# Kernel optimization log

Measured on AMD Instinct MI355X. Metric: run time of the kernel, lower is better.

## Reference

```python
import jax, jax.numpy as jnp
import numpy as np

N_NODES = 100000


def gcn_conv(x, edge_src, edge_dst, W, b):
    # PyG GCNConv: h = x @ W; add self-loops; symmetric normalization; scatter-add; + bias
    n = x.shape[0]
    h = x @ W  # [N, out]
    loop = jnp.arange(n, dtype=edge_src.dtype)
    src = jnp.concatenate([edge_src, loop])
    dst = jnp.concatenate([edge_dst, loop])
    deg = jax.ops.segment_sum(jnp.ones_like(dst, dtype=h.dtype), dst, num_segments=n)
    dinv = jnp.where(deg > 0, jax.lax.rsqrt(deg), 0.0)
    norm = dinv[src] * dinv[dst]  # [E+N]
    msg = h[src] * norm[:, None]  # gather + scale
    out = jax.ops.segment_sum(msg, dst, num_segments=n)  # scatter-add
    return out + b


def setup_inputs() -> dict:
    key = jax.random.key(0)
    ks = jax.random.split(key, 12)
    F_in, H, H2, C = 128, 64, 32, 2
    x = jax.random.normal(ks[0], (N_NODES, F_in), dtype=jnp.float32)
    edge_index = jax.random.randint(ks[1], (2, 3200000), 0, N_NODES, dtype=jnp.int64)
    def glorot(k, shape):
        lim = float(np.sqrt(6.0 / (shape[0] + shape[1])))
        return jax.random.uniform(k, shape, jnp.float32, -lim, lim)
    return {
        "x": x,
        "edge_index": edge_index,
        "W1": glorot(ks[2], (F_in, H)), "b1": jnp.zeros((H,), jnp.float32),
        "W2": glorot(ks[3], (H, H)), "b2": jnp.zeros((H,), jnp.float32),
        "Wl1": glorot(ks[4], (H, H2)), "bl1": jnp.zeros((H2,), jnp.float32),
        "Wl2": glorot(ks[5], (H2, C)), "bl2": jnp.zeros((C,), jnp.float32),
    }


def reference(x, edge_index, W1, b1, W2, b2, Wl1, bl1, Wl2, bl2):
    src, dst = edge_index[0], edge_index[1]
    h = gcn_conv(x, src, dst, W1, b1)
    h = jax.nn.relu(h)
    # dropout is identity in eval mode (training=self.training)
    h = gcn_conv(h, src, dst, W2, b2)
    h = h @ Wl1 + bl1
    h = h @ Wl2 + bl2
    return jax.nn.softmax(h, axis=0)
```

## Files before the change

### kernel.cpp

```cpp
#include <hip/hip_runtime.h>

#define F_IN 128
#define NBMAX 512
#define TILE1 8192
#define CAP   9472
#define CAP2  10240

typedef __attribute__((ext_vector_type(8))) short short8;
typedef __attribute__((ext_vector_type(4))) float f32x4;
typedef __attribute__((ext_vector_type(2))) float f32x2;

__device__ __forceinline__ unsigned short f2bf(float f) {
    unsigned u = __float_as_uint(f);
    u += 0x7fffu + ((u >> 16) & 1u);
    return (unsigned short)(u >> 16);
}

__device__ __forceinline__ unsigned char f2fp8(float f) {
    return (unsigned char)(__builtin_amdgcn_cvt_pk_fp8_f32(f, f, 0, false) & 0xff);
}

__device__ __forceinline__ unsigned ldG(const unsigned* __restrict__ G,
                                        unsigned c, unsigned sl) {
    return *(const unsigned*)((const char*)G + ((c << 6) + (sl << 2)));
}

__global__ __launch_bounds__(1024) void k_part1(const int* __restrict__ src,
                                                const int* __restrict__ dst,
                                                int* __restrict__ cursor,
                                                unsigned* __restrict__ ebuf,
                                                int E, int nb) {
    __shared__ unsigned staged[TILE1];
    __shared__ unsigned short sbuck[TILE1];
    __shared__ int hist[NBMAX], lbase[NBMAX], lcur[NBMAX], gbase[NBMAX];
    int t = threadIdx.x;
    for (int i = t; i < nb; i += 1024) hist[i] = 0;
    __syncthreads();
    int base = blockIdx.x * TILE1;
    int end = min(base + TILE1, E);
    for (int i = base + t; i < end; i += 1024)
        atomicAdd(&hist[dst[i] >> 8], 1);
    __syncthreads();
    if (t < 64) {
        int carry = 0;
        for (int c = 0; c < (nb + 63) / 64; ++c) {
            int idx = c * 64 + t;
            int v = (idx < nb) ? hist[idx] : 0;
            int inc = v;
            for (int d = 1; d < 64; d <<= 1) {
                int u = __shfl_up(inc, d, 64);
                if (t >= d) inc += u;
            }
            if (idx < nb) { int ex = carry + inc - v; lbase[idx] = ex; lcur[idx] = ex; }
            carry += __shfl(inc, 63, 64);
        }
    }
    __syncthreads();
    for (int i = t; i < nb; i += 1024)
        gbase[i] = i * CAP + (hist[i] ? atomicAdd(&cursor[i], hist[i]) : 0);
    for (int i = base + t; i < end; i += 1024) {
        int d = dst[i];
        int b = d >> 8;
        int r = atomicAdd(&lcur[b], 1);
        staged[r] = ((unsigned)src[i] << 8) | (unsigned)(d & 255);
        sbuck[r] = (unsigned short)b;
    }
    __syncthreads();
    int cnt = end - base;
    for (int i = t; i < cnt; i += 1024) {
        int b = sbuck[i];
        __builtin_nontemporal_store(staged[i], &ebuf[gbase[b] + (i - lbase[b])]);
    }
}

__global__ __launch_bounds__(1024) void k_part2(const unsigned* __restrict__ ebuf,
                                                const int* __restrict__ cursor,
                                                int* __restrict__ csr,
                                                uint2* __restrict__ offs2,
                                                float* __restrict__ dinv, int n) {
    __shared__ unsigned staged[CAP2];
    __shared__ int hist[256], lcur[256];
    int t = threadIdx.x;
    int b = blockIdx.x;
    int beg = b * CAP;
    int cnt = cursor[b];
    int end = beg + cnt;
    if (t < 256) hist[t] = 0;
    __syncthreads();
    for (int i = beg + t; i < end; i += 1024)
        atomicAdd(&hist[ebuf[i] & 255u], 1);
    __syncthreads();
    if (t < 64) {
        int carry = 0;
        for (int c = 0; c < 4; ++c) {
            int idx = c * 64 + t;
            int v = hist[idx];
            int inc = v;
            for (int d = 1; d < 64; d <<= 1) {
                int u = __shfl_up(inc, d, 64);
                if (t >= d) inc += u;
            }
            int ex = carry + inc - v;
            lcur[idx] = ex;
            int node = b * 256 + idx;
            if (node < n) {
                offs2[node] = make_uint2((unsigned)(beg + ex), (unsigned)(beg + ex + v));
                dinv[node] = rsqrtf((float)(v + 1));
            }
            carry += __shfl(inc, 63, 64);
        }
    }
    __syncthreads();
    for (int i = beg + t; i < end; i += 1024) {
        unsigned e = __builtin_nontemporal_load(ebuf + i);
        int r = atomicAdd(&lcur[(int)(e & 255u)], 1);
        staged[r] = e >> 8;
    }
    __syncthreads();
    for (int i = t; i < cnt; i += 1024)
        csr[beg + i] = (int)staged[i];
    if (t < 64) csr[end + t] = n;
}

template<int K, bool INBF16>
__global__ __launch_bounds__(256) void k_gemm_mfma(const void* __restrict__ Xv,
                                                   const float* __restrict__ W,
                                                   const float* __restrict__ dinv,
                                                   unsigned* __restrict__ G, int n,
                                                   const float* __restrict__ W2,
                                                   const float* __restrict__ b2,
                                                   const float* __restrict__ Wl1,
                                                   const float* __restrict__ bl1,
                                                   const float* __restrict__ Wl2,
                                                   const float* __restrict__ bl2,
                                                   float* __restrict__ Wfold,
                                                   float* __restrict__ bconst) {
    constexpr int AST = K + 8;
    __shared__ unsigned short A_lds[64 * AST];
    __shared__ unsigned short Wt_lds[64 * AST];
    __shared__ unsigned char C8[64 * 68];
    __shared__ float Wc[64][2];
    __shared__ float bc0[2];
    int t = threadIdx.x;
    int base = blockIdx.x * 64;

    if (blockIdx.x == 0) {
        if (t < 128) {
            int k = t >> 1, c = t & 1;
            float s = 0.f;
            for (int m = 0; m < 32; ++m) s += Wl1[k * 32 + m] * Wl2[m * 2 + c];
            Wc[k][c] = s;
        } else if (t < 130) {
            int c = t - 128;
            float s = bl2[c];
            for (int m = 0; m < 32; ++m) s += bl1[m] * Wl2[m * 2 + c];
            bc0[c] = s;
        } else if (t >= 240 && t < 256) {
            G[(size_t)n * 16 + (t - 240)] = 0u;
        }
        __syncthreads();
        if (t < 128) {
            int k = t >> 1, c = t & 1;
            float s = 0.f;
            for (int j = 0; j < 64; ++j) s += W2[k * 64 + j] * Wc[j][c];
            Wfold[k * 2 + c] = s;
        } else if (t < 130) {
            int c = t - 128;
            float s = bc0[c];
            for (int j = 0; j < 64; ++j) s += b2[j] * Wc[j][c];
            bconst[c] = s;
        }
    }

    for (int idx = t; idx < K * 64; idx += 256) {
        int k = idx >> 6, nn = idx & 63;
        Wt_lds[nn * AST + k] = f2bf(W[idx]);
    }
    if (!INBF16) {
        const f32x4* X4 = (const f32x4*)Xv;
        constexpr int F4 = K / 4;
        for (int idx = t; idx < 64 * F4; idx += 256) {
            int row = idx / F4, c4 = idx % F4;
            f32x4 f = {0.f, 0.f, 0.f, 0.f};
            if (base + row < n) f = X4[(size_t)base * F4 + idx];
            unsigned p0 = (unsigned)f2bf(f.x) | ((unsigned)f2bf(f.y) << 16);
            unsigned p1 = (unsigned)f2bf(f.z) | ((unsigned)f2bf(f.w) << 16);
            *(uint2*)&A_lds[row * AST + c4 * 4] = make_uint2(p0, p1);
        }
    } else {
        const unsigned* H32 = (const unsigned*)Xv;
        constexpr int U2 = K / 2;
        for (int idx = t; idx < 64 * U2; idx += 256) {
            int row = idx / U2, c2 = idx % U2;
            unsigned u = 0;
            if (base + row < n) u = H32[(size_t)base * U2 + idx];
            *(unsigned*)&A_lds[row * AST + c2 * 2] = u;
        }
    }
    __syncthreads();

    int lane = t & 63, w = t >> 6;
    int q = lane >> 4, m = lane & 15;
    f32x4 acc0 = {0,0,0,0}, acc1 = {0,0,0,0}, acc2 = {0,0,0,0}, acc3 = {0,0,0,0};
    const unsigned short* arow = &A_lds[(16 * w + m) * AST + q * 8];
#pragma unroll
    for (int s = 0; s < K / 32; ++s) {
        short8 a  = *(const short8*)(arow + s * 32);
        short8 w0 = *(const short8*)&Wt_lds[ m       * AST + s * 32 + q * 8];
        short8 w1 = *(const short8*)&Wt_lds[(16 + m) * AST + s * 32 + q * 8];
        short8 w2 = *(const short8*)&Wt_lds[(32 + m) * AST + s * 32 + q * 8];
        short8 w3 = *(const short8*)&Wt_lds[(48 + m) * AST + s * 32 + q * 8];
        acc0 = __builtin_amdgcn_mfma_f32_16x16x32_bf16(a, w0, acc0, 0, 0, 0);
        acc1 = __builtin_amdgcn_mfma_f32_16x16x32_bf16(a, w1, acc1, 0, 0, 0);
        acc2 = __builtin_amdgcn_mfma_f32_16x16x32_bf16(a, w2, acc2, 0, 0, 0);
        acc3 = __builtin_amdgcn_mfma_f32_16x16x32_bf16(a, w3, acc3, 0, 0, 0);
    }
    float dv[4];
#pragma unroll
    for (int r = 0; r < 4; ++r) {
        int node = base + 16 * w + q * 4 + r;
        dv[r] = (node < n) ? dinv[node] : 0.f;
    }
#pragma unroll
    for (int r = 0; r < 4; ++r) {
        int row = 16 * w + q * 4 + r;
        C8[row * 68 + m]      = f2fp8(acc0[r] * dv[r]);
        C8[row * 68 + 16 + m] = f2fp8(acc1[r] * dv[r]);
        C8[row * 68 + 32 + m] = f2fp8(acc2[r] * dv[r]);
        C8[row * 68 + 48 + m] = f2fp8(acc3[r] * dv[r]);
    }
    __syncthreads();
    for (int idx = t; idx < 1024; idx += 256) {
        int row = idx >> 4, c4 = idx & 15;
        int node = base + row;
        if (node < n) G[(size_t)node * 16 + c4] = *(const unsigned*)&C8[row * 68 + c4 * 4];
    }
}

__global__ __launch_bounds__(256) void k_gfold(const int* __restrict__ csr,
                                               const uint2* __restrict__ offs2,
                                               const unsigned* __restrict__ G,
                                               const float* __restrict__ dinv,
                                               const float* __restrict__ bias,
                                               const float* __restrict__ Wfold,
                                               float2* __restrict__ P, int n) {
    int w = (blockIdx.x * 256 + threadIdx.x) >> 6;
    if (w >= n) return;
    int lane = threadIdx.x & 63;
    unsigned g = (unsigned)lane >> 4, sl = (unsigned)lane & 15u;
    uint2 o = offs2[w];
    int beg = (int)o.x, end = (int)o.y;
    f32x2 A01 = {0.f, 0.f}, A23 = {0.f, 0.f};

    unsigned selfU = ldG(G, (unsigned)w, sl);
    for (int e = beg; e < end; e += 64) {
        int i0 = e + (int)g;
        int vv[16];
#pragma unroll
        for (int k = 0; k < 16; ++k)
            vv[k] = csr[i0 + 4 * k];
        unsigned uu[16];
#pragma unroll
        for (int k = 0; k < 16; ++k) {
            unsigned c = (i0 + 4 * k < end) ? (unsigned)vv[k] : (unsigned)n;
            uu[k] = ldG(G, c, sl);
        }
#pragma unroll
        for (int k = 0; k < 16; ++k) {
            A01 += __builtin_amdgcn_cvt_pk_f32_fp8((int)uu[k], false);
            A23 += __builtin_amdgcn_cvt_pk_f32_fp8((int)uu[k], true);
        }
    }
    float a0 = A01.x, a1 = A01.y, a2 = A23.x, a3 = A23.y;
    a0 += __shfl_xor(a0, 16, 64); a1 += __shfl_xor(a1, 16, 64);
    a2 += __shfl_xor(a2, 16, 64); a3 += __shfl_xor(a3, 16, 64);
    a0 += __shfl_xor(a0, 32, 64); a1 += __shfl_xor(a1, 32, 64);
    a2 += __shfl_xor(a2, 32, 64); a3 += __shfl_xor(a3, 32, 64);
    A01 = __builtin_amdgcn_cvt_pk_f32_fp8((int)selfU, false);
    A23 = __builtin_amdgcn_cvt_pk_f32_fp8((int)selfU, true);
    a0 += A01.x; a1 += A01.y; a2 += A23.x; a3 += A23.y;
    float d = dinv[w];
    float4 bb = ((const float4*)bias)[sl];
    float v0 = fmaxf(fmaf(a0, d, bb.x), 0.f);
    float v1 = fmaxf(fmaf(a1, d, bb.y), 0.f);
    float v2 = fmaxf(fmaf(a2, d, bb.z), 0.f);
    float v3 = fmaxf(fmaf(a3, d, bb.w), 0.f);
    float4 wa = ((const float4*)Wfold)[2 * sl];
    float4 wb = ((const float4*)Wfold)[2 * sl + 1];
    float px = v0 * wa.x + v1 * wa.z + v2 * wb.x + v3 * wb.z;
    float py = v0 * wa.y + v1 * wa.w + v2 * wb.y + v3 * wb.w;
    px += __shfl_xor(px, 1, 64); py += __shfl_xor(py, 1, 64);
    px += __shfl_xor(px, 2, 64); py += __shfl_xor(py, 2, 64);
    px += __shfl_xor(px, 4, 64); py += __shfl_xor(py, 4, 64);
    px += __shfl_xor(px, 8, 64); py += __shfl_xor(py, 8, 64);
    if (lane == 0) P[w] = make_float2(px * d, py * d);
}

__global__ __launch_bounds__(256) void k_gather2(const int* __restrict__ csr,
                                                 const uint2* __restrict__ offs2,
                                                 const float2* __restrict__ P,
                                                 const float* __restrict__ dinv,
                                                 const float* __restrict__ bconst,
                                                 float* __restrict__ logits, int n) {
    int w = (blockIdx.x * 256 + threadIdx.x) >> 4;
    if (w >= n) return;
    int sl = threadIdx.x & 15;
    uint2 o = offs2[w];
    int beg = (int)o.x, end = (int)o.y;
    float ax = 0.f, ay = 0.f;
    for (int e = beg; e < end; e += 64) {
        int i0 = e + sl;
        int vv[4];
#pragma unroll
        for (int k = 0; k < 4; ++k)
            vv[k] = csr[i0 + 16 * k];
#pragma unroll
        for (int k = 0; k < 4; ++k) {
            unsigned j = (i0 + 16 * k < end) ? (unsigned)vv[k] : (unsigned)n;
            float2 p = *(const float2*)((const char*)P + (j << 3));
            ax += p.x; ay += p.y;
        }
    }
    ax += __shfl_xor(ax, 1, 64); ay += __shfl_xor(ay, 1, 64);
    ax += __shfl_xor(ax, 2, 64); ay += __shfl_xor(ay, 2, 64);
    ax += __shfl_xor(ax, 4, 64); ay += __shfl_xor(ay, 4, 64);
    ax += __shfl_xor(ax, 8, 64); ay += __shfl_xor(ay, 8, 64);
    if (sl == 0) {
        float2 self = P[w];
        float d = dinv[w];
        logits[w * 2]     = d * (self.x + ax) + bconst[0];
        logits[w * 2 + 1] = d * (self.y + ay) + bconst[1];
    }
}

__global__ __launch_bounds__(256) void k_sm_part(const float* __restrict__ logits,
                                                 float4* __restrict__ partials, int n) {
    __shared__ float r0[256], r1[256];
    int t = threadIdx.x;
    int i = blockIdx.x * 256 + t;
    float l0 = -3.4e38f, l1 = -3.4e38f;
    if (i < n) { l0 = logits[i * 2]; l1 = logits[i * 2 + 1]; }
    r0[t] = l0; r1[t] = l1;
    __syncthreads();
    for (int s = 128; s > 0; s >>= 1) {
        if (t < s) { r0[t] = fmaxf(r0[t], r0[t + s]); r1[t] = fmaxf(r1[t], r1[t + s]); }
        __syncthreads();
    }
    float m0 = r0[0], m1 = r1[0];
    __syncthreads();
    r0[t] = (i < n) ? __expf(l0 - m0) : 0.f;
    r1[t] = (i < n) ? __expf(l1 - m1) : 0.f;
    __syncthreads();
    for (int s = 128; s > 0; s >>= 1) {
        if (t < s) { r0[t] += r0[t + s]; r1[t] += r1[t + s]; }
        __syncthreads();
    }
    if (t == 0) partials[blockIdx.x] = make_float4(m0, r0[0], m1, r1[0]);
}

__global__ __launch_bounds__(256) void k_sm_final(const float* __restrict__ logits,
                                                  const float4* __restrict__ partials,
                                                  float* __restrict__ out, int n, int nbp) {
    __shared__ float m0s[256], s0s[256], m1s[256], s1s[256];
    int t = threadIdx.x;
    float m0 = -3.4e38f, s0 = 0.f, m1 = -3.4e38f, s1 = 0.f;
    for (int i = t; i < nbp; i += 256) {
        float4 p = partials[i];
        float M = fmaxf(m0, p.x);
        s0 = s0 * __expf(m0 - M) + p.y * __expf(p.x - M); m0 = M;
        M = fmaxf(m1, p.z);
        s1 = s1 * __expf(m1 - M) + p.w * __expf(p.z - M); m1 = M;
    }
    m0s[t] = m0; s0s[t] = s0; m1s[t] = m1; s1s[t] = s1;
    __syncthreads();
    for (int s = 128; s > 0; s >>= 1) {
        if (t < s) {
            float Ma = m0s[t], Mb = m0s[t + s];
            float M = fmaxf(Ma, Mb);
            s0s[t] = s0s[t] * __expf(Ma - M) + s0s[t + s] * __expf(Mb - M);
            m0s[t] = M;
            Ma = m1s[t]; Mb = m1s[t + s];
            M = fmaxf(Ma, Mb);
            s1s[t] = s1s[t] * __expf(Ma - M) + s1s[t + s] * __expf(Mb - M);
            m1s[t] = M;
        }
        __syncthreads();
    }
    float M0 = m0s[0], inv0 = 1.f / s0s[0];
    float M1 = m1s[0], inv1 = 1.f / s1s[0];
    int i = blockIdx.x * 256 + t;
    if (i < n) {
        out[i * 2]     = __expf(logits[i * 2]     - M0) * inv0;
        out[i * 2 + 1] = __expf(logits[i * 2 + 1] - M1) * inv1;
    }
}

extern "C" void kernel_launch(void* const* d_in, const int* in_sizes, int n_in,
                              void* d_out, int out_size, void* d_ws, size_t ws_size,
                              hipStream_t stream) {
    const float* x   = (const float*)d_in[0];
    const int*   ei  = (const int*)d_in[1];
    const float* W1  = (const float*)d_in[2];
    const float* b1  = (const float*)d_in[3];
    const float* W2  = (const float*)d_in[4];
    const float* b2  = (const float*)d_in[5];
    const float* Wl1 = (const float*)d_in[6];
    const float* bl1 = (const float*)d_in[7];
    const float* Wl2 = (const float*)d_in[8];
    const float* bl2 = (const float*)d_in[9];
    float* out = (float*)d_out;

    int N = in_sizes[0] / F_IN;
    int E = in_sizes[1] / 2;
    const int* esrc = ei;
    const int* edst = ei + E;

    int nbuck = (N + 255) / 256;

    char* ws = (char*)d_ws;
    size_t off = 0;
    auto alloc = [&](size_t bytes) { void* p = ws + off; off += (bytes + 255) & ~(size_t)255; return p; };
    int*            cursor = (int*)alloc((size_t)NBMAX * 4);
    float*          dinv   = (float*)alloc((size_t)N * 4);
    uint2*          offs2  = (uint2*)alloc((size_t)N * 8);
    int*            csr    = (int*)alloc((size_t)nbuck * CAP * 4);
    unsigned*       ebuf   = (unsigned*)alloc((size_t)nbuck * CAP * 4);
    unsigned*       gbuf   = (unsigned*)alloc((size_t)(N + 1) * 64);
    float*          Wfold  = (float*)alloc(64 * 2 * 4);
    float*          bconst = (float*)alloc(2 * 4);
    float2*         P      = (float2*)alloc((size_t)(N + 1) * 8);
    float*          logits = (float*)alloc((size_t)N * 2 * 4);
    float4*         smpart = (float4*)alloc((size_t)NBMAX * 16);

    hipMemsetAsync(cursor, 0, NBMAX * sizeof(int), stream);
    hipMemsetAsync(P + N, 0, sizeof(float2), stream);

    int tiles = (E + TILE1 - 1) / TILE1;
    int mb = (N + 63) / 64;
    int wb = (N * 64 + 255) / 256;
    int qb = (N * 16 + 255) / 256;
    int nb = (N + 255) / 256;

    k_part1<<<tiles, 1024, 0, stream>>>(esrc, edst, cursor, ebuf, E, nbuck);
    k_part2<<<nbuck, 1024, 0, stream>>>(ebuf, cursor, csr, offs2, dinv, N);

    k_gemm_mfma<128, false><<<mb, 256, 0, stream>>>(x, W1, dinv, gbuf, N,
                                                    W2, b2, Wl1, bl1, Wl2, bl2,
                                                    Wfold, bconst);

    k_gfold<<<wb, 256, 0, stream>>>(csr, offs2, gbuf, dinv, b1, Wfold, P, N);

    k_gather2<<<qb, 256, 0, stream>>>(csr, offs2, P, dinv, bconst, logits, N);

    k_sm_part<<<nb, 256, 0, stream>>>(logits, smpart, N);
    k_sm_final<<<nb, 256, 0, stream>>>(logits, smpart, out, N, nb);
}
```

Baseline: 223.9 us.

## Pad CSR rows to multiples of 64 with sentinel indices to drop bounds checks

Result: slower. 232.0 us (+3.6%).

```diff
diff --git a/kernel.cpp b/kernel.cpp
--- a/kernel.cpp
+++ b/kernel.cpp
@@ -4,7 +4,7 @@
 #define NBMAX 512
 #define TILE1 8192
 #define CAP   9472
-#define CAP2  10240
+#define CAPC  16896
 
 typedef __attribute__((ext_vector_type(8))) short short8;
 typedef __attribute__((ext_vector_type(4))) float f32x4;
@@ -78,11 +78,13 @@
                                                 int* __restrict__ csr,
                                                 uint2* __restrict__ offs2,
                                                 float* __restrict__ dinv, int n) {
-    __shared__ unsigned staged[CAP2];
+    __shared__ int staged[CAPC];
     __shared__ int hist[256], lcur[256];
+    __shared__ int sh_ptot;
     int t = threadIdx.x;
     int b = blockIdx.x;
     int beg = b * CAP;
+    int cbase = b * CAPC;
     int cnt = cursor[b];
     int end = beg + cnt;
     if (t < 256) hist[t] = 0;
@@ -95,31 +97,37 @@
         for (int c = 0; c < 4; ++c) {
             int idx = c * 64 + t;
             int v = hist[idx];
-            int inc = v;
+            int pd = (v + 63) & ~63;
+            int inc = pd;
             for (int d = 1; d < 64; d <<= 1) {
                 int u = __shfl_up(inc, d, 64);
                 if (t >= d) inc += u;
             }
-            int ex = carry + inc - v;
+            int ex = carry + inc - pd;
             lcur[idx] = ex;
             int node = b * 256 + idx;
             if (node < n) {
-                offs2[node] = make_uint2((unsigned)(beg + ex), (unsigned)(beg + ex + v));
+                offs2[node] = make_uint2((unsigned)(cbase + ex),
+                                         (unsigned)(cbase + ex + pd));
                 dinv[node] = rsqrtf((float)(v + 1));
             }
             carry += __shfl(inc, 63, 64);
         }
-    }
-    __syncthreads();
+        if (t == 0) sh_ptot = carry;
+    } else {
+        for (int i = t - 64; i < CAPC; i += 960) staged[i] = n;
+    }
+    __syncthreads();
+    if (t < 64) {  }
     for (int i = beg + t; i < end; i += 1024) {
         unsigned e = __builtin_nontemporal_load(ebuf + i);
         int r = atomicAdd(&lcur[(int)(e & 255u)], 1);
-        staged[r] = e >> 8;
-    }
-    __syncthreads();
-    for (int i = t; i < cnt; i += 1024)
-        csr[beg + i] = (int)staged[i];
-    if (t < 64) csr[end + t] = n;
+        staged[r] = (int)(e >> 8);
+    }
+    __syncthreads();
+    int ptot = sh_ptot;
+    for (int i = t; i < ptot; i += 1024)
+        csr[cbase + i] = staged[i];
 }
 
 template<int K, bool INBF16>
@@ -249,22 +257,16 @@
     int lane = threadIdx.x & 63;
     unsigned g = (unsigned)lane >> 4, sl = (unsigned)lane & 15u;
     uint2 o = offs2[w];
-    int beg = (int)o.x, end = (int)o.y;
+    int beg = (int)o.x, pend = (int)o.y;
     f32x2 A01 = {0.f, 0.f}, A23 = {0.f, 0.f};
 
     unsigned selfU = ldG(G, (unsigned)w, sl);
-    for (int e = beg; e < end; e += 64) {
+    for (int e = beg; e < pend; e += 64) {
         int i0 = e + (int)g;
-        int vv[16];
+        unsigned uu[16];
 #pragma unroll
         for (int k = 0; k < 16; ++k)
-            vv[k] = csr[i0 + 4 * k];
-        unsigned uu[16];
-#pragma unroll
-        for (int k = 0; k < 16; ++k) {
-            unsigned c = (i0 + 4 * k < end) ? (unsigned)vv[k] : (unsigned)n;
-            uu[k] = ldG(G, c, sl);
-        }
+            uu[k] = ldG(G, (unsigned)csr[i0 + 4 * k], sl);
 #pragma unroll
         for (int k = 0; k < 16; ++k) {
             A01 += __builtin_amdgcn_cvt_pk_f32_fp8((int)uu[k], false);
@@ -306,17 +308,13 @@
     if (w >= n) return;
     int sl = threadIdx.x & 15;
     uint2 o = offs2[w];
-    int beg = (int)o.x, end = (int)o.y;
+    int beg = (int)o.x, pend = (int)o.y;
     float ax = 0.f, ay = 0.f;
-    for (int e = beg; e < end; e += 64) {
+    for (int e = beg; e < pend; e += 64) {
         int i0 = e + sl;
-        int vv[4];
-#pragma unroll
-        for (int k = 0; k < 4; ++k)
-            vv[k] = csr[i0 + 16 * k];
 #pragma unroll
         for (int k = 0; k < 4; ++k) {
-            unsigned j = (i0 + 16 * k < end) ? (unsigned)vv[k] : (unsigned)n;
+            unsigned j = (unsigned)csr[i0 + 16 * k];
             float2 p = *(const float2*)((const char*)P + (j << 3));
             ax += p.x; ay += p.y;
         }
@@ -423,7 +421,7 @@
     int*            cursor = (int*)alloc((size_t)NBMAX * 4);
     float*          dinv   = (float*)alloc((size_t)N * 4);
     uint2*          offs2  = (uint2*)alloc((size_t)N * 8);
-    int*            csr    = (int*)alloc((size_t)nbuck * CAP * 4);
+    int*            csr    = (int*)alloc((size_t)nbuck * CAPC * 4);
     unsigned*       ebuf   = (unsigned*)alloc((size_t)nbuck * CAP * 4);
     unsigned*       gbuf   = (unsigned*)alloc((size_t)(N + 1) * 64);
     float*          Wfold  = (float*)alloc(64 * 2 * 4);
```

## Shrink partition buckets and fuse softmax partial reduction into gather kernel

Applied to the files above, without the earlier changes.

New measurement: 241.5 us. +7.9%, slower.

```diff
diff --git a/kernel.cpp b/kernel.cpp
--- a/kernel.cpp
+++ b/kernel.cpp
@@ -1,10 +1,9 @@
 #include <hip/hip_runtime.h>
 
 #define F_IN 128
-#define NBMAX 512
-#define TILE1 8192
-#define CAP   9472
-#define CAP2  10240
+#define NBMAX 1024
+#define TILE1 4096
+#define CAPB  4800
 
 typedef __attribute__((ext_vector_type(8))) short short8;
 typedef __attribute__((ext_vector_type(4))) float f32x4;
@@ -25,21 +24,28 @@
     return *(const unsigned*)((const char*)G + ((c << 6) + (sl << 2)));
 }
 
-__global__ __launch_bounds__(1024) void k_part1(const int* __restrict__ src,
-                                                const int* __restrict__ dst,
-                                                int* __restrict__ cursor,
-                                                unsigned* __restrict__ ebuf,
-                                                int E, int nb) {
+__global__ __launch_bounds__(512) void k_part1(const int* __restrict__ src,
+                                               const int* __restrict__ dst,
+                                               int* __restrict__ cursor,
+                                               unsigned* __restrict__ ebuf,
+                                               int E, int nb) {
     __shared__ unsigned staged[TILE1];
     __shared__ unsigned short sbuck[TILE1];
     __shared__ int hist[NBMAX], lbase[NBMAX], lcur[NBMAX], gbase[NBMAX];
     int t = threadIdx.x;
-    for (int i = t; i < nb; i += 1024) hist[i] = 0;
+    for (int i = t; i < nb; i += 512) hist[i] = 0;
     __syncthreads();
     int base = blockIdx.x * TILE1;
     int end = min(base + TILE1, E);
-    for (int i = base + t; i < end; i += 1024)
-        atomicAdd(&hist[dst[i] >> 8], 1);
+    int dreg[8];
+#pragma unroll
+    for (int k = 0; k < 8; ++k) {
+        int i = base + t + 512 * k;
+        dreg[k] = (i < end) ? dst[i] : -1;
+    }
+#pragma unroll
+    for (int k = 0; k < 8; ++k)
+        if (dreg[k] >= 0) atomicAdd(&hist[dreg[k] >> 7], 1);
     __syncthreads();
     if (t < 64) {
         int carry = 0;
@@ -56,43 +62,46 @@
         }
     }
     __syncthreads();
-    for (int i = t; i < nb; i += 1024)
-        gbase[i] = i * CAP + (hist[i] ? atomicAdd(&cursor[i], hist[i]) : 0);
-    for (int i = base + t; i < end; i += 1024) {
-        int d = dst[i];
-        int b = d >> 8;
-        int r = atomicAdd(&lcur[b], 1);
-        staged[r] = ((unsigned)src[i] << 8) | (unsigned)(d & 255);
-        sbuck[r] = (unsigned short)b;
+    for (int i = t; i < nb; i += 512)
+        gbase[i] = i * CAPB + (hist[i] ? atomicAdd(&cursor[i], hist[i]) : 0);
+#pragma unroll
+    for (int k = 0; k < 8; ++k) {
+        if (dreg[k] < 0) continue;
+        int i = base + t + 512 * k;
+        int d = dreg[k];
+        int bb = d >> 7;
+        int r = atomicAdd(&lcur[bb], 1);
+        staged[r] = ((unsigned)src[i] << 8) | (unsigned)(d & 127);
+        sbuck[r] = (unsigned short)bb;
     }
     __syncthreads();
     int cnt = end - base;
-    for (int i = t; i < cnt; i += 1024) {
-        int b = sbuck[i];
-        __builtin_nontemporal_store(staged[i], &ebuf[gbase[b] + (i - lbase[b])]);
-    }
-}
-
-__global__ __launch_bounds__(1024) void k_part2(const unsigned* __restrict__ ebuf,
-                                                const int* __restrict__ cursor,
-                                                int* __restrict__ csr,
-                                                uint2* __restrict__ offs2,
-                                                float* __restrict__ dinv, int n) {
-    __shared__ unsigned staged[CAP2];
-    __shared__ int hist[256], lcur[256];
+    for (int i = t; i < cnt; i += 512) {
+        int bb = sbuck[i];
+        ebuf[gbase[bb] + (i - lbase[bb])] = staged[i];
+    }
+}
+
+__global__ __launch_bounds__(512) void k_part2(const unsigned* __restrict__ ebuf,
+                                               const int* __restrict__ cursor,
+                                               int* __restrict__ csr,
+                                               uint2* __restrict__ offs2,
+                                               float* __restrict__ dinv, int n) {
+    __shared__ int staged[CAPB];
+    __shared__ int hist[128], lcur[128];
     int t = threadIdx.x;
     int b = blockIdx.x;
-    int beg = b * CAP;
+    int beg = b * CAPB;
     int cnt = cursor[b];
     int end = beg + cnt;
-    if (t < 256) hist[t] = 0;
-    __syncthreads();
-    for (int i = beg + t; i < end; i += 1024)
-        atomicAdd(&hist[ebuf[i] & 255u], 1);
+    if (t < 128) hist[t] = 0;
+    __syncthreads();
+    for (int i = beg + t; i < end; i += 512)
+        atomicAdd(&hist[ebuf[i] & 127u], 1);
     __syncthreads();
     if (t < 64) {
         int carry = 0;
-        for (int c = 0; c < 4; ++c) {
+        for (int c = 0; c < 2; ++c) {
             int idx = c * 64 + t;
             int v = hist[idx];
             int inc = v;
@@ -102,7 +111,7 @@
             }
             int ex = carry + inc - v;
             lcur[idx] = ex;
-            int node = b * 256 + idx;
+            int node = b * 128 + idx;
             if (node < n) {
                 offs2[node] = make_uint2((unsigned)(beg + ex), (unsigned)(beg + ex + v));
                 dinv[node] = rsqrtf((float)(v + 1));
@@ -111,14 +120,14 @@
         }
     }
     __syncthreads();
-    for (int i = beg + t; i < end; i += 1024) {
-        unsigned e = __builtin_nontemporal_load(ebuf + i);
-        int r = atomicAdd(&lcur[(int)(e & 255u)], 1);
-        staged[r] = e >> 8;
-    }
-    __syncthreads();
-    for (int i = t; i < cnt; i += 1024)
-        csr[beg + i] = (int)staged[i];
+    for (int i = beg + t; i < end; i += 512) {
+        unsigned e = ebuf[i];
+        int r = atomicAdd(&lcur[(int)(e & 127u)], 1);
+        staged[r] = (int)(e >> 8);
+    }
+    __syncthreads();
+    for (int i = t; i < cnt; i += 512)
+        csr[beg + i] = staged[i];
     if (t < 64) csr[end + t] = n;
 }
 
@@ -301,11 +310,15 @@
                                                  const float2* __restrict__ P,
                                                  const float* __restrict__ dinv,
                                                  const float* __restrict__ bconst,
-                                                 float* __restrict__ logits, int n) {
-    int w = (blockIdx.x * 256 + threadIdx.x) >> 4;
-    if (w >= n) return;
-    int sl = threadIdx.x & 15;
-    uint2 o = offs2[w];
+                                                 float* __restrict__ logits,
+                                                 float4* __restrict__ partials, int n) {
+    __shared__ float sml[16][2];
+    int t = threadIdx.x;
+    int w = (blockIdx.x * 256 + t) >> 4;
+    int sl = t & 15;
+    int grp = t >> 4;
+    bool valid = (w < n);
+    uint2 o = valid ? offs2[w] : make_uint2(0u, 0u);
     int beg = (int)o.x, end = (int)o.y;
     float ax = 0.f, ay = 0.f;
     for (int e = beg; e < end; e += 64) {
@@ -325,37 +338,34 @@
     ax += __shfl_xor(ax, 2, 64); ay += __shfl_xor(ay, 2, 64);
     ax += __shfl_xor(ax, 4, 64); ay += __shfl_xor(ay, 4, 64);
     ax += __shfl_xor(ax, 8, 64); ay += __shfl_xor(ay, 8, 64);
-    if (sl == 0) {
+    float l0 = -3.4e38f, l1 = -3.4e38f;
+    if (valid && sl == 0) {
         float2 self = P[w];
         float d = dinv[w];
-        logits[w * 2]     = d * (self.x + ax) + bconst[0];
-        logits[w * 2 + 1] = d * (self.y + ay) + bconst[1];
-    }
-}
-
-__global__ __launch_bounds__(256) void k_sm_part(const float* __restrict__ logits,
-                                                 float4* __restrict__ partials, int n) {
-    __shared__ float r0[256], r1[256];
-    int t = threadIdx.x;
-    int i = blockIdx.x * 256 + t;
-    float l0 = -3.4e38f, l1 = -3.4e38f;
-    if (i < n) { l0 = logits[i * 2]; l1 = logits[i * 2 + 1]; }
-    r0[t] = l0; r1[t] = l1;
-    __syncthreads();
-    for (int s = 128; s > 0; s >>= 1) {
-        if (t < s) { r0[t] = fmaxf(r0[t], r0[t + s]); r1[t] = fmaxf(r1[t], r1[t + s]); }
-        __syncthreads();
-    }
-    float m0 = r0[0], m1 = r1[0];
-    __syncthreads();
-    r0[t] = (i < n) ? __expf(l0 - m0) : 0.f;
-    r1[t] = (i < n) ? __expf(l1 - m1) : 0.f;
-    __syncthreads();
-    for (int s = 128; s > 0; s >>= 1) {
-        if (t < s) { r0[t] += r0[t + s]; r1[t] += r1[t + s]; }
-        __syncthreads();
-    }
-    if (t == 0) partials[blockIdx.x] = make_float4(m0, r0[0], m1, r1[0]);
+        l0 = d * (self.x + ax) + bconst[0];
+        l1 = d * (self.y + ay) + bconst[1];
+        logits[w * 2]     = l0;
+        logits[w * 2 + 1] = l1;
+    }
+    if (sl == 0) { sml[grp][0] = l0; sml[grp][1] = l1; }
+    __syncthreads();
+    if (t < 16) {
+        float a = sml[t][0], bv = sml[t][1];
+        float m0 = a, m1 = bv;
+#pragma unroll
+        for (int d = 1; d < 16; d <<= 1) {
+            m0 = fmaxf(m0, __shfl_xor(m0, d, 64));
+            m1 = fmaxf(m1, __shfl_xor(m1, d, 64));
+        }
+        float e0 = (a > -1e38f) ? __expf(a - m0) : 0.f;
+        float e1 = (bv > -1e38f) ? __expf(bv - m1) : 0.f;
+#pragma unroll
+        for (int d = 1; d < 16; d <<= 1) {
+            e0 += __shfl_xor(e0, d, 64);
+            e1 += __shfl_xor(e1, d, 64);
+        }
+        if (t == 0) partials[blockIdx.x] = make_float4(m0, e0, m1, e1);
+    }
 }
 
 __global__ __launch_bounds__(256) void k_sm_final(const float* __restrict__ logits,
@@ -415,7 +425,7 @@
     const int* esrc = ei;
     const int* edst = ei + E;
 
-    int nbuck = (N + 255) / 256;
+    int nbuck = (N + 127) / 128;
 
     char* ws = (char*)d_ws;
     size_t off = 0;
@@ -423,14 +433,15 @@
     int*            cursor = (int*)alloc((size_t)NBMAX * 4);
     float*          dinv   = (float*)alloc((size_t)N * 4);
     uint2*          offs2  = (uint2*)alloc((size_t)N * 8);
-    int*            csr    = (int*)alloc((size_t)nbuck * CAP * 4);
-    unsigned*       ebuf   = (unsigned*)alloc((size_t)nbuck * CAP * 4);
+    int*            csr    = (int*)alloc((size_t)nbuck * CAPB * 4);
+    unsigned*       ebuf   = (unsigned*)alloc((size_t)nbuck * CAPB * 4);
     unsigned*       gbuf   = (unsigned*)alloc((size_t)(N + 1) * 64);
     float*          Wfold  = (float*)alloc(64 * 2 * 4);
     float*          bconst = (float*)alloc(2 * 4);
     float2*         P      = (float2*)alloc((size_t)(N + 1) * 8);
     float*          logits = (float*)alloc((size_t)N * 2 * 4);
-    float4*         smpart = (float4*)alloc((size_t)NBMAX * 16);
+    int qb = (N * 16 + 255) / 256;
+    float4*         partials = (float4*)alloc((size_t)qb * 16);
 
     hipMemsetAsync(cursor, 0, NBMAX * sizeof(int), stream);
     hipMemsetAsync(P + N, 0, sizeof(float2), stream);
@@ -438,11 +449,10 @@
     int tiles = (E + TILE1 - 1) / TILE1;
     int mb = (N + 63) / 64;
     int wb = (N * 64 + 255) / 256;
-    int qb = (N * 16 + 255) / 256;
     int nb = (N + 255) / 256;
 
-    k_part1<<<tiles, 1024, 0, stream>>>(esrc, edst, cursor, ebuf, E, nbuck);
-    k_part2<<<nbuck, 1024, 0, stream>>>(ebuf, cursor, csr, offs2, dinv, N);
+    k_part1<<<tiles, 512, 0, stream>>>(esrc, edst, cursor, ebuf, E, nbuck);
+    k_part2<<<nbuck, 512, 0, stream>>>(ebuf, cursor, csr, offs2, dinv, N);
 
     k_gemm_mfma<128, false><<<mb, 256, 0, stream>>>(x, W1, dinv, gbuf, N,
                                                     W2, b2, Wl1, bl1, Wl2, bl2,
@@ -450,8 +460,7 @@
 
     k_gfold<<<wb, 256, 0, stream>>>(csr, offs2, gbuf, dinv, b1, Wfold, P, N);
 
-    k_gather2<<<qb, 256, 0, stream>>>(csr, offs2, P, dinv, bconst, logits, N);
-
-    k_sm_part<<<nb, 256, 0, stream>>>(logits, smpart, N);
-    k_sm_final<<<nb, 256, 0, stream>>>(logits, smpart, out, N, nb);
-}
+    k_gather2<<<qb, 256, 0, stream>>>(csr, offs2, P, dinv, bconst, logits, partials, N);
+
+    k_sm_final<<<nb, 256, 0, stream>>>(logits, partials, out, N, qb);
+}
```

## Split layer-1 gather into two feature halves and fuse softmax partials into gather2

Applied to the files above, without the earlier changes.

Result: slower. 257.4 us (+15.0%).

```diff
diff --git a/kernel.cpp b/kernel.cpp
--- a/kernel.cpp
+++ b/kernel.cpp
@@ -15,14 +15,16 @@
     u += 0x7fffu + ((u >> 16) & 1u);
     return (unsigned short)(u >> 16);
 }
+__device__ __forceinline__ float bflo(unsigned u) { return __uint_as_float(u << 16); }
+__device__ __forceinline__ float bfhi(unsigned u) { return __uint_as_float(u & 0xffff0000u); }
 
 __device__ __forceinline__ unsigned char f2fp8(float f) {
     return (unsigned char)(__builtin_amdgcn_cvt_pk_fp8_f32(f, f, 0, false) & 0xff);
 }
 
-__device__ __forceinline__ unsigned ldG(const unsigned* __restrict__ G,
-                                        unsigned c, unsigned sl) {
-    return *(const unsigned*)((const char*)G + ((c << 6) + (sl << 2)));
+__device__ __forceinline__ unsigned ldGH(const unsigned* __restrict__ G,
+                                         unsigned c, unsigned sl) {
+    return *(const unsigned*)((const char*)G + ((c << 5) + (sl << 2)));
 }
 
 __global__ __launch_bounds__(1024) void k_part1(const int* __restrict__ src,
@@ -38,8 +40,15 @@
     __syncthreads();
     int base = blockIdx.x * TILE1;
     int end = min(base + TILE1, E);
-    for (int i = base + t; i < end; i += 1024)
-        atomicAdd(&hist[dst[i] >> 8], 1);
+    int dreg[8];
+#pragma unroll
+    for (int k = 0; k < 8; ++k) {
+        int i = base + t + 1024 * k;
+        dreg[k] = (i < end) ? dst[i] : -1;
+    }
+#pragma unroll
+    for (int k = 0; k < 8; ++k)
+        if (dreg[k] >= 0) atomicAdd(&hist[dreg[k] >> 8], 1);
     __syncthreads();
     if (t < 64) {
         int carry = 0;
@@ -58,8 +67,11 @@
     __syncthreads();
     for (int i = t; i < nb; i += 1024)
         gbase[i] = i * CAP + (hist[i] ? atomicAdd(&cursor[i], hist[i]) : 0);
-    for (int i = base + t; i < end; i += 1024) {
-        int d = dst[i];
+#pragma unroll
+    for (int k = 0; k < 8; ++k) {
+        if (dreg[k] < 0) continue;
+        int i = base + t + 1024 * k;
+        int d = dreg[k];
         int b = d >> 8;
         int r = atomicAdd(&lcur[b], 1);
         staged[r] = ((unsigned)src[i] << 8) | (unsigned)(d & 255);
@@ -126,7 +138,8 @@
 __global__ __launch_bounds__(256) void k_gemm_mfma(const void* __restrict__ Xv,
                                                    const float* __restrict__ W,
                                                    const float* __restrict__ dinv,
-                                                   unsigned* __restrict__ G, int n,
+                                                   unsigned* __restrict__ GA,
+                                                   unsigned* __restrict__ GB, int n,
                                                    const float* __restrict__ W2,
                                                    const float* __restrict__ b2,
                                                    const float* __restrict__ Wl1,
@@ -134,7 +147,8 @@
                                                    const float* __restrict__ Wl2,
                                                    const float* __restrict__ bl2,
                                                    float* __restrict__ Wfold,
-                                                   float* __restrict__ bconst) {
+                                                   float* __restrict__ bconst,
+                                                   float2* __restrict__ P) {
     constexpr int AST = K + 8;
     __shared__ unsigned short A_lds[64 * AST];
     __shared__ unsigned short Wt_lds[64 * AST];
@@ -155,8 +169,12 @@
             float s = bl2[c];
             for (int m = 0; m < 32; ++m) s += bl1[m] * Wl2[m * 2 + c];
             bc0[c] = s;
-        } else if (t >= 240 && t < 256) {
-            G[(size_t)n * 16 + (t - 240)] = 0u;
+        } else if (t == 200) {
+            P[n] = make_float2(0.f, 0.f);
+        } else if (t >= 240 && t < 248) {
+            GA[(size_t)n * 8 + (t - 240)] = 0u;
+        } else if (t >= 248) {
+            GB[(size_t)n * 8 + (t - 248)] = 0u;
         }
         __syncthreads();
         if (t < 128) {
@@ -233,66 +251,127 @@
     for (int idx = t; idx < 1024; idx += 256) {
         int row = idx >> 4, c4 = idx & 15;
         int node = base + row;
-        if (node < n) G[(size_t)node * 16 + c4] = *(const unsigned*)&C8[row * 68 + c4 * 4];
-    }
-}
-
-__global__ __launch_bounds__(256) void k_gfold(const int* __restrict__ csr,
-                                               const uint2* __restrict__ offs2,
-                                               const unsigned* __restrict__ G,
-                                               const float* __restrict__ dinv,
-                                               const float* __restrict__ bias,
-                                               const float* __restrict__ Wfold,
-                                               float2* __restrict__ P, int n) {
+        if (node < n) {
+            unsigned v = *(const unsigned*)&C8[row * 68 + c4 * 4];
+            if (c4 < 8) GA[(size_t)node * 8 + c4] = v;
+            else        GB[(size_t)node * 8 + (c4 - 8)] = v;
+        }
+    }
+}
+
+__global__ __launch_bounds__(256) void k_gfoldA(const int* __restrict__ csr,
+                                                const uint2* __restrict__ offs2,
+                                                const unsigned* __restrict__ GA,
+                                                uint2* __restrict__ HA, int n) {
     int w = (blockIdx.x * 256 + threadIdx.x) >> 6;
     if (w >= n) return;
     int lane = threadIdx.x & 63;
-    unsigned g = (unsigned)lane >> 4, sl = (unsigned)lane & 15u;
+    unsigned g = (unsigned)lane >> 3, sl = (unsigned)lane & 7u;
     uint2 o = offs2[w];
     int beg = (int)o.x, end = (int)o.y;
     f32x2 A01 = {0.f, 0.f}, A23 = {0.f, 0.f};
-
-    unsigned selfU = ldG(G, (unsigned)w, sl);
+    unsigned selfU = ldGH(GA, (unsigned)w, sl);
     for (int e = beg; e < end; e += 64) {
         int i0 = e + (int)g;
-        int vv[16];
-#pragma unroll
-        for (int k = 0; k < 16; ++k)
-            vv[k] = csr[i0 + 4 * k];
-        unsigned uu[16];
-#pragma unroll
-        for (int k = 0; k < 16; ++k) {
-            unsigned c = (i0 + 4 * k < end) ? (unsigned)vv[k] : (unsigned)n;
-            uu[k] = ldG(G, c, sl);
-        }
-#pragma unroll
-        for (int k = 0; k < 16; ++k) {
+        int vv[8];
+#pragma unroll
+        for (int k = 0; k < 8; ++k)
+            vv[k] = csr[i0 + 8 * k];
+        unsigned uu[8];
+#pragma unroll
+        for (int k = 0; k < 8; ++k) {
+            unsigned c = (i0 + 8 * k < end) ? (unsigned)vv[k] : (unsigned)n;
+            uu[k] = ldGH(GA, c, sl);
+        }
+#pragma unroll
+        for (int k = 0; k < 8; ++k) {
             A01 += __builtin_amdgcn_cvt_pk_f32_fp8((int)uu[k], false);
             A23 += __builtin_amdgcn_cvt_pk_f32_fp8((int)uu[k], true);
         }
     }
     float a0 = A01.x, a1 = A01.y, a2 = A23.x, a3 = A23.y;
-    a0 += __shfl_xor(a0, 16, 64); a1 += __shfl_xor(a1, 16, 64);
-    a2 += __shfl_xor(a2, 16, 64); a3 += __shfl_xor(a3, 16, 64);
-    a0 += __shfl_xor(a0, 32, 64); a1 += __shfl_xor(a1, 32, 64);
-    a2 += __shfl_xor(a2, 32, 64); a3 += __shfl_xor(a3, 32, 64);
-    A01 = __builtin_amdgcn_cvt_pk_f32_fp8((int)selfU, false);
-    A23 = __builtin_amdgcn_cvt_pk_f32_fp8((int)selfU, true);
-    a0 += A01.x; a1 += A01.y; a2 += A23.x; a3 += A23.y;
+#pragma unroll
+    for (int m = 8; m <= 32; m <<= 1) {
+        a0 += __shfl_xor(a0, m, 64); a1 += __shfl_xor(a1, m, 64);
+        a2 += __shfl_xor(a2, m, 64); a3 += __shfl_xor(a3, m, 64);
+    }
+    f32x2 s0 = __builtin_amdgcn_cvt_pk_f32_fp8((int)selfU, false);
+    f32x2 s1 = __builtin_amdgcn_cvt_pk_f32_fp8((int)selfU, true);
+    a0 += s0.x; a1 += s0.y; a2 += s1.x; a3 += s1.y;
+    if (g == 0) {
+        unsigned p0 = (unsigned)f2bf(a0) | ((unsigned)f2bf(a1) << 16);
+        unsigned p1 = (unsigned)f2bf(a2) | ((unsigned)f2bf(a3) << 16);
+        HA[(size_t)w * 8 + sl] = make_uint2(p0, p1);
+    }
+}
+
+__global__ __launch_bounds__(256) void k_gfoldB(const int* __restrict__ csr,
+                                                const uint2* __restrict__ offs2,
+                                                const unsigned* __restrict__ GB,
+                                                const uint2* __restrict__ HA,
+                                                const float* __restrict__ dinv,
+                                                const float* __restrict__ bias,
+                                                const float* __restrict__ Wfold,
+                                                float2* __restrict__ P, int n) {
+    int w = (blockIdx.x * 256 + threadIdx.x) >> 6;
+    if (w >= n) return;
+    int lane = threadIdx.x & 63;
+    unsigned g = (unsigned)lane >> 3, sl = (unsigned)lane & 7u;
+    uint2 o = offs2[w];
+    int beg = (int)o.x, end = (int)o.y;
+    f32x2 B01 = {0.f, 0.f}, B23 = {0.f, 0.f};
+    unsigned selfU = ldGH(GB, (unsigned)w, sl);
+    for (int e = beg; e < end; e += 64) {
+        int i0 = e + (int)g;
+        int vv[8];
+#pragma unroll
+        for (int k = 0; k < 8; ++k)
+            vv[k] = csr[i0 + 8 * k];
+        unsigned uu[8];
+#pragma unroll
+        for (int k = 0; k < 8; ++k) {
+            unsigned c = (i0 + 8 * k < end) ? (unsigned)vv[k] : (unsigned)n;
+            uu[k] = ldGH(GB, c, sl);
+        }
+#pragma unroll
+        for (int k = 0; k < 8; ++k) {
+            B01 += __builtin_amdgcn_cvt_pk_f32_fp8((int)uu[k], false);
+            B23 += __builtin_amdgcn_cvt_pk_f32_fp8((int)uu[k], true);
+        }
+    }
+    float b0 = B01.x, b1v = B01.y, b2v = B23.x, b3 = B23.y;
+#pragma unroll
+    for (int m = 8; m <= 32; m <<= 1) {
+        b0 += __shfl_xor(b0, m, 64); b1v += __shfl_xor(b1v, m, 64);
+        b2v += __shfl_xor(b2v, m, 64); b3 += __shfl_xor(b3, m, 64);
+    }
+    f32x2 s0 = __builtin_amdgcn_cvt_pk_f32_fp8((int)selfU, false);
+    f32x2 s1 = __builtin_amdgcn_cvt_pk_f32_fp8((int)selfU, true);
+    b0 += s0.x; b1v += s0.y; b2v += s1.x; b3 += s1.y;
+    uint2 h = HA[(size_t)w * 8 + sl];
+    float a0 = bflo(h.x), a1 = bfhi(h.x), a2 = bflo(h.y), a3 = bfhi(h.y);
     float d = dinv[w];
-    float4 bb = ((const float4*)bias)[sl];
-    float v0 = fmaxf(fmaf(a0, d, bb.x), 0.f);
-    float v1 = fmaxf(fmaf(a1, d, bb.y), 0.f);
-    float v2 = fmaxf(fmaf(a2, d, bb.z), 0.f);
-    float v3 = fmaxf(fmaf(a3, d, bb.w), 0.f);
-    float4 wa = ((const float4*)Wfold)[2 * sl];
-    float4 wb = ((const float4*)Wfold)[2 * sl + 1];
-    float px = v0 * wa.x + v1 * wa.z + v2 * wb.x + v3 * wb.z;
-    float py = v0 * wa.y + v1 * wa.w + v2 * wb.y + v3 * wb.w;
+    float4 bA = ((const float4*)bias)[sl];
+    float4 bB = ((const float4*)bias)[8 + sl];
+    float v0 = fmaxf(fmaf(a0, d, bA.x), 0.f);
+    float v1 = fmaxf(fmaf(a1, d, bA.y), 0.f);
+    float v2 = fmaxf(fmaf(a2, d, bA.z), 0.f);
+    float v3 = fmaxf(fmaf(a3, d, bA.w), 0.f);
+    float v4 = fmaxf(fmaf(b0, d, bB.x), 0.f);
+    float v5 = fmaxf(fmaf(b1v, d, bB.y), 0.f);
+    float v6 = fmaxf(fmaf(b2v, d, bB.z), 0.f);
+    float v7 = fmaxf(fmaf(b3, d, bB.w), 0.f);
+    float4 wa0 = ((const float4*)Wfold)[2 * sl];
+    float4 wa1 = ((const float4*)Wfold)[2 * sl + 1];
+    float4 wb0 = ((const float4*)Wfold)[16 + 2 * sl];
+    float4 wb1 = ((const float4*)Wfold)[16 + 2 * sl + 1];
+    float px = v0 * wa0.x + v1 * wa0.z + v2 * wa1.x + v3 * wa1.z
+             + v4 * wb0.x + v5 * wb0.z + v6 * wb1.x + v7 * wb1.z;
+    float py = v0 * wa0.y + v1 * wa0.w + v2 * wa1.y + v3 * wa1.w
+             + v4 * wb0.y + v5 * wb0.w + v6 * wb1.y + v7 * wb1.w;
     px += __shfl_xor(px, 1, 64); py += __shfl_xor(py, 1, 64);
     px += __shfl_xor(px, 2, 64); py += __shfl_xor(py, 2, 64);
     px += __shfl_xor(px, 4, 64); py += __shfl_xor(py, 4, 64);
-    px += __shfl_xor(px, 8, 64); py += __shfl_xor(py, 8, 64);
     if (lane == 0) P[w] = make_float2(px * d, py * d);
 }
 
@@ -301,11 +380,15 @@
                                                  const float2* __restrict__ P,
                                                  const float* __restrict__ dinv,
                                                  const float* __restrict__ bconst,
-                                                 float* __restrict__ logits, int n) {
-    int w = (blockIdx.x * 256 + threadIdx.x) >> 4;
-    if (w >= n) return;
-    int sl = threadIdx.x & 15;
-    uint2 o = offs2[w];
+                                                 float* __restrict__ logits,
+                                                 float4* __restrict__ partials, int n) {
+    __shared__ float sml[16][2];
+    int t = threadIdx.x;
+    int w = (blockIdx.x * 256 + t) >> 4;
+    int sl = t & 15;
+    int grp = t >> 4;
+    bool valid = (w < n);
+    uint2 o = valid ? offs2[w] : make_uint2(0u, 0u);
     int beg = (int)o.x, end = (int)o.y;
     float ax = 0.f, ay = 0.f;
     for (int e = beg; e < end; e += 64) {
@@ -325,37 +408,34 @@
     ax += __shfl_xor(ax, 2, 64); ay += __shfl_xor(ay, 2, 64);
     ax += __shfl_xor(ax, 4, 64); ay += __shfl_xor(ay, 4, 64);
     ax += __shfl_xor(ax, 8, 64); ay += __shfl_xor(ay, 8, 64);
-    if (sl == 0) {
+    float l0 = -3.4e38f, l1 = -3.4e38f;
+    if (valid && sl == 0) {
         float2 self = P[w];
         float d = dinv[w];
-        logits[w * 2]     = d * (self.x + ax) + bconst[0];
-        logits[w * 2 + 1] = d * (self.y + ay) + bconst[1];
-    }
-}
-
-__global__ __launch_bounds__(256) void k_sm_part(const float* __restrict__ logits,
-                                                 float4* __restrict__ partials, int n) {
-    __shared__ float r0[256], r1[256];
-    int t = threadIdx.x;
-    int i = blockIdx.x * 256 + t;
-    float l0 = -3.4e38f, l1 = -3.4e38f;
-    if (i < n) { l0 = logits[i * 2]; l1 = logits[i * 2 + 1]; }
-    r0[t] = l0; r1[t] = l1;
-    __syncthreads();
-    for (int s = 128; s > 0; s >>= 1) {
-        if (t < s) { r0[t] = fmaxf(r0[t], r0[t + s]); r1[t] = fmaxf(r1[t], r1[t + s]); }
-        __syncthreads();
-    }
-    float m0 = r0[0], m1 = r1[0];
-    __syncthreads();
-    r0[t] = (i < n) ? __expf(l0 - m0) : 0.f;
-    r1[t] = (i < n) ? __expf(l1 - m1) : 0.f;
-    __syncthreads();
-    for (int s = 128; s > 0; s >>= 1) {
-        if (t < s) { r0[t] += r0[t + s]; r1[t] += r1[t + s]; }
-        __syncthreads();
-    }
-    if (t == 0) partials[blockIdx.x] = make_float4(m0, r0[0], m1, r1[0]);
+        l0 = d * (self.x + ax) + bconst[0];
+        l1 = d * (self.y + ay) + bconst[1];
+        logits[w * 2]     = l0;
+        logits[w * 2 + 1] = l1;
+    }
+    if (sl == 0) { sml[grp][0] = l0; sml[grp][1] = l1; }
+    __syncthreads();
+    if (t < 16) {
+        float a = sml[t][0], bv = sml[t][1];
+        float m0 = a, m1 = bv;
+#pragma unroll
+        for (int d = 1; d < 16; d <<= 1) {
+            m0 = fmaxf(m0, __shfl_xor(m0, d, 64));
+            m1 = fmaxf(m1, __shfl_xor(m1, d, 64));
+        }
+        float e0 = (a > -1e38f) ? __expf(a - m0) : 0.f;
+        float e1 = (bv > -1e38f) ? __expf(bv - m1) : 0.f;
+#pragma unroll
+        for (int d = 1; d < 16; d <<= 1) {
+            e0 += __shfl_xor(e0, d, 64);
+            e1 += __shfl_xor(e1, d, 64);
+        }
+        if (t == 0) partials[blockIdx.x] = make_float4(m0, e0, m1, e1);
+    }
 }
 
 __global__ __launch_bounds__(256) void k_sm_final(const float* __restrict__ logits,
@@ -425,33 +505,34 @@
     uint2*          offs2  = (uint2*)alloc((size_t)N * 8);
     int*            csr    = (int*)alloc((size_t)nbuck * CAP * 4);
     unsigned*       ebuf   = (unsigned*)alloc((size_t)nbuck * CAP * 4);
-    unsigned*       gbuf   = (unsigned*)alloc((size_t)(N + 1) * 64);
+    unsigned*       GA     = (unsigned*)alloc((size_t)(N + 1) * 32);
+    unsigned*       GB     = (unsigned*)alloc((size_t)(N + 1) * 32);
+    uint2*          HA     = (uint2*)alloc((size_t)N * 64);
     float*          Wfold  = (float*)alloc(64 * 2 * 4);
     float*          bconst = (float*)alloc(2 * 4);
     float2*         P      = (float2*)alloc((size_t)(N + 1) * 8);
     float*          logits = (float*)alloc((size_t)N * 2 * 4);
-    float4*         smpart = (float4*)alloc((size_t)NBMAX * 16);
+    int qb = (N * 16 + 255) / 256;
+    float4*         partials = (float4*)alloc((size_t)qb * 16);
 
     hipMemsetAsync(cursor, 0, NBMAX * sizeof(int), stream);
-    hipMemsetAsync(P + N, 0, sizeof(float2), stream);
 
     int tiles = (E + TILE1 - 1) / TILE1;
     int mb = (N + 63) / 64;
     int wb = (N * 64 + 255) / 256;
-    int qb = (N * 16 + 255) / 256;
     int nb = (N + 255) / 256;
 
     k_part1<<<tiles, 1024, 0, stream>>>(esrc, edst, cursor, ebuf, E, nbuck);
     k_part2<<<nbuck, 1024, 0, stream>>>(ebuf, cursor, csr, offs2, dinv, N);
 
-    k_gemm_mfma<128, false><<<mb, 256, 0, stream>>>(x, W1, dinv, gbuf, N,
+    k_gemm_mfma<128, false><<<mb, 256, 0, stream>>>(x, W1, dinv, GA, GB, N,
                                                     W2, b2, Wl1, bl1, Wl2, bl2,
-                                                    Wfold, bconst);
-
-    k_gfold<<<wb, 256, 0, stream>>>(csr, offs2, gbuf, dinv, b1, Wfold, P, N);
-
-    k_gather2<<<qb, 256, 0, stream>>>(csr, offs2, P, dinv, bconst, logits, N);
-
-    k_sm_part<<<nb, 256, 0, stream>>>(logits, smpart, N);
-    k_sm_final<<<nb, 256, 0, stream>>>(logits, smpart, out, N, nb);
-}
+                                                    Wfold, bconst, P);
+
+    k_gfoldA<<<wb, 256, 0, stream>>>(csr, offs2, GA, HA, N);
+    k_gfoldB<<<wb, 256, 0, stream>>>(csr, offs2, GB, HA, dinv, b1, Wfold, P, N);
+
+    k_gather2<<<qb, 256, 0, stream>>>(csr, offs2, P, dinv, bconst, logits, partials, N);
+
+    k_sm_final<<<nb, 256, 0, stream>>>(logits, partials, out, N, qb);
+}
```
